# Kernel tuning notes

Measured on AMD Instinct MI355X. Metric: run time of the kernel, lower is better.

The kernel has to match this reference:

```python
import jax, jax.numpy as jnp
import numpy as np

PATCH = 32
K_FILT = 4
B, NP, C = 32, 256, 3


def _dct_matrix(n):
    i = np.arange(n)[:, None]
    j = np.arange(n)[None, :]
    scale = np.where(i == 0, np.sqrt(1.0 / n), np.sqrt(2.0 / n))
    m = scale * np.cos((j + 0.5) * np.pi * i / n)
    return jnp.asarray(m, dtype=jnp.float32)


def _bandpass_filters(n, k_filt):
    i = np.arange(n)[:, None]
    j = np.arange(n)[None, :]
    s = i + j  # [n, n]
    ks = np.arange(k_filt)[:, None, None]
    lo = 2.0 * n / k_filt * ks
    hi = 2.0 * n / k_filt * (ks + 1)
    f = ((s >= lo) & (s < hi)).astype(np.float32)  # [K, n, n]
    return jnp.asarray(f)


def setup_inputs() -> dict:
    key = jax.random.key(0)
    x = jax.random.normal(key, (B, NP, C, PATCH, PATCH), dtype=jnp.float32)
    return {
        'x': x,
        'dct_matrix': _dct_matrix(PATCH),
        'bandpass_filters': _bandpass_filters(PATCH, K_FILT),
    }


def reference(x, dct_matrix, bandpass_filters):
    # Batched 2D DCT: D @ patch @ D^T for every (b, n, c) patch.
    dct_coeffs = jnp.einsum('ih,bnchw,jw->bncij', dct_matrix, x, dct_matrix)
    log_abs = jnp.log1p(jnp.abs(dct_coeffs))  # log(|X| + 1)
    # patch_score = sum_k sum_c 2^k * (log_abs[c] * filter_k).sum()
    k_weights = 2.0 ** jnp.arange(bandpass_filters.shape[0], dtype=jnp.float32)
    weight_map = jnp.einsum('k,khw->hw', k_weights, bandpass_filters)  # [H, W]
    patch_grades = jnp.einsum('bnchw,hw->bn', log_abs, weight_map)
    return dct_coeffs, patch_grades
```

## Files before the change

kernel.cpp:

```cpp
#include <hip/hip_runtime.h>

#define NPIX 1024
#define CH   3
#define PPB  2
#define WVS  (PPB * CH)
#define BLK  (WVS * 64)

__global__ __launch_bounds__(BLK) void dct_grade_kernel(
    const float* __restrict__ x,
    const float* __restrict__ dct,
    float* __restrict__ out_coeffs,
    float* __restrict__ out_grades)
{
    __shared__ __align__(16) float Dt[NPIX];
    __shared__ __align__(16) float S[WVS][NPIX];
    __shared__ float partial[WVS];

    const int tid  = threadIdx.x;
    const int wid  = tid >> 6;
    const int lane = tid & 63;

    if (tid < 256) {
        int i  = tid & 31;
        int h0 = (tid >> 5) << 2;
        float4 dv = *reinterpret_cast<const float4*>(dct + i * 32 + h0);
        Dt[(h0 + 0) * 32 + i] = dv.x;
        Dt[(h0 + 1) * 32 + i] = dv.y;
        Dt[(h0 + 2) * 32 + i] = dv.z;
        Dt[(h0 + 3) * 32 + i] = dv.w;
    }
    __syncthreads();

    const int p  = (wid >= CH) ? 1 : 0;
    const int c  = wid - CH * p;
    const int pn = blockIdx.x * PPB + p;

    const int i0 = (lane >> 3) << 2;
    const int c0 = (lane & 7) << 2;
    const int sw = i0 ^ ((lane & 7) << 2);

    float* Sw = &S[wid][0];
    const float* xg   = x          + (size_t)pn * (CH * NPIX) + c * NPIX;
    float*       outp = out_coeffs + (size_t)pn * (CH * NPIX) + c * NPIX;

    {
        const float4* src = reinterpret_cast<const float4*>(xg);
        float4*       dst = reinterpret_cast<float4*>(Sw);
        #pragma unroll
        for (int k = 0; k < 4; ++k)
            dst[lane + 64 * k] = src[lane + 64 * k];
    }

    float acc[4][4];
    #pragma unroll
    for (int a = 0; a < 4; ++a)
        #pragma unroll
        for (int b = 0; b < 4; ++b) acc[a][b] = 0.0f;

    #pragma unroll
    for (int h = 0; h < 32; ++h) {
        float4 dv = *reinterpret_cast<const float4*>(&Dt[h * 32 + i0]);
        float4 xv = *reinterpret_cast<const float4*>(&Sw[h * 32 + c0]);
        float da[4] = {dv.x, dv.y, dv.z, dv.w};
        float xa[4] = {xv.x, xv.y, xv.z, xv.w};
        #pragma unroll
        for (int ii = 0; ii < 4; ++ii)
            #pragma unroll
            for (int ww = 0; ww < 4; ++ww)
                acc[ii][ww] += da[ii] * xa[ww];
    }

    #pragma unroll
    for (int ww = 0; ww < 4; ++ww) {
        float4 col = make_float4(acc[0][ww], acc[1][ww], acc[2][ww], acc[3][ww]);
        *reinterpret_cast<float4*>(&Sw[(c0 + ww) * 32 + sw]) = col;
    }

    float y[4][4];
    #pragma unroll
    for (int a = 0; a < 4; ++a)
        #pragma unroll
        for (int b = 0; b < 4; ++b) y[a][b] = 0.0f;

    #pragma unroll
    for (int w = 0; w < 32; ++w) {
        float4 tv = *reinterpret_cast<const float4*>(&Sw[w * 32 + (i0 ^ ((w >> 2) << 2))]);
        float4 dv = *reinterpret_cast<const float4*>(&Dt[w * 32 + c0]);
        float ta[4] = {tv.x, tv.y, tv.z, tv.w};
        float da[4] = {dv.x, dv.y, dv.z, dv.w};
        #pragma unroll
        for (int ii = 0; ii < 4; ++ii)
            #pragma unroll
            for (int jj = 0; jj < 4; ++jj)
                y[ii][jj] += ta[ii] * da[jj];
    }

    const int ssum = i0 + c0;
    float g = 0.0f;
    #pragma unroll
    for (int ii = 0; ii < 4; ++ii) {
        float4 st = make_float4(y[ii][0], y[ii][1], y[ii][2], y[ii][3]);
        *reinterpret_cast<float4*>(&outp[(i0 + ii) * 32 + c0]) = st;
        #pragma unroll
        for (int jj = 0; jj < 4; ++jj) {
            float wgt = (float)(1 << ((ssum + ii + jj) >> 4));
            g += __logf(1.0f + fabsf(y[ii][jj])) * wgt;
        }
    }

    #pragma unroll
    for (int off = 32; off > 0; off >>= 1)
        g += __shfl_down(g, off);
    if (lane == 0) partial[wid] = g;
    __syncthreads();
    if (tid < PPB)
        out_grades[blockIdx.x * PPB + tid] =
            partial[tid * CH + 0] + partial[tid * CH + 1] + partial[tid * CH + 2];
}

extern "C" void kernel_launch(void* const* d_in, const int* in_sizes, int n_in,
                              void* d_out, int out_size, void* d_ws, size_t ws_size,
                              hipStream_t stream) {
    const float* x   = (const float*)d_in[0];
    const float* dct = (const float*)d_in[1];
    float* out_coeffs = (float*)d_out;
    float* out_grades = (float*)d_out + (size_t)8192 * CH * NPIX;

    dct_grade_kernel<<<8192 / PPB, BLK, 0, stream>>>(x, dct, out_coeffs, out_grades);
}
```

Baseline: 190.0 us.

## Compute DCT per half-wave with register columns and padded LDS transpose

Each half-wave now handles one 32x32 channel slice: each lane loads one column of x into registers, computes the first DCT pass with DCT coefficients read from global memory (wave-uniform, likely scalar loads), and writes the result to an LDS tile padded to 33 columns. It then reads a row back and computes the second pass. The goal is to double the slices per block, drop the LDS staging of x and of the DCT matrix, and avoid bank conflicts. In exchange it uses more registers (64+ floats per lane), and the global stores become strided per-row float4 writes, which coalesce less well.

After: 220.4 us. 1.16x slower.

```diff
diff --git a/kernel.cpp b/kernel.cpp
--- a/kernel.cpp
+++ b/kernel.cpp
@@ -1,10 +1,11 @@
 #include <hip/hip_runtime.h>
 
-#define NPIX 1024
-#define CH   3
-#define PPB  2
-#define WVS  (PPB * CH)
-#define BLK  (WVS * 64)
+#define NPIX   1024
+#define CH     3
+#define WAVES  6
+#define SLICES (WAVES * 2)
+#define BLK    (WAVES * 64)
+#define LDP    33
 
 __global__ __launch_bounds__(BLK) void dct_grade_kernel(
     const float* __restrict__ x,
@@ -12,109 +13,80 @@
     float* __restrict__ out_coeffs,
     float* __restrict__ out_grades)
 {
-    __shared__ __align__(16) float Dt[NPIX];
-    __shared__ __align__(16) float S[WVS][NPIX];
-    __shared__ float partial[WVS];
+    __shared__ float T[SLICES][32 * LDP];
+    __shared__ float partial[SLICES];
 
     const int tid  = threadIdx.x;
     const int wid  = tid >> 6;
     const int lane = tid & 63;
+    const int half = lane >> 5;
+    const int t    = lane & 31;
 
-    if (tid < 256) {
-        int i  = tid & 31;
-        int h0 = (tid >> 5) << 2;
-        float4 dv = *reinterpret_cast<const float4*>(dct + i * 32 + h0);
-        Dt[(h0 + 0) * 32 + i] = dv.x;
-        Dt[(h0 + 1) * 32 + i] = dv.y;
-        Dt[(h0 + 2) * 32 + i] = dv.z;
-        Dt[(h0 + 3) * 32 + i] = dv.w;
-    }
-    __syncthreads();
+    const int slot = wid * 2 + half;
+    const int s    = blockIdx.x * SLICES + slot;
 
-    const int p  = (wid >= CH) ? 1 : 0;
-    const int c  = wid - CH * p;
-    const int pn = blockIdx.x * PPB + p;
+    const float* xg   = x          + (size_t)s * NPIX;
+    float*       outp = out_coeffs + (size_t)s * NPIX;
 
-    const int i0 = (lane >> 3) << 2;
-    const int c0 = (lane & 7) << 2;
-    const int sw = i0 ^ ((lane & 7) << 2);
+    float xcol[32];
+    #pragma unroll
+    for (int h = 0; h < 32; ++h)
+        xcol[h] = xg[h * 32 + t];
 
-    float* Sw = &S[wid][0];
-    const float* xg   = x          + (size_t)pn * (CH * NPIX) + c * NPIX;
-    float*       outp = out_coeffs + (size_t)pn * (CH * NPIX) + c * NPIX;
+    float* Tw = &T[slot][0];
 
-    {
-        const float4* src = reinterpret_cast<const float4*>(xg);
-        float4*       dst = reinterpret_cast<float4*>(Sw);
+    #pragma unroll
+    for (int i = 0; i < 32; ++i) {
+        const float* dr = dct + i * 32;
+        float p0 = 0.f, p1 = 0.f, p2 = 0.f, p3 = 0.f;
         #pragma unroll
-        for (int k = 0; k < 4; ++k)
-            dst[lane + 64 * k] = src[lane + 64 * k];
+        for (int h = 0; h < 32; h += 4) {
+            p0 += dr[h + 0] * xcol[h + 0];
+            p1 += dr[h + 1] * xcol[h + 1];
+            p2 += dr[h + 2] * xcol[h + 2];
+            p3 += dr[h + 3] * xcol[h + 3];
+        }
+        Tw[i * LDP + t] = (p0 + p1) + (p2 + p3);
     }
 
-    float acc[4][4];
+    float trow[32];
     #pragma unroll
-    for (int a = 0; a < 4; ++a)
-        #pragma unroll
-        for (int b = 0; b < 4; ++b) acc[a][b] = 0.0f;
+    for (int w = 0; w < 32; ++w)
+        trow[w] = Tw[t * LDP + w];
 
+    float g = 0.f;
     #pragma unroll
-    for (int h = 0; h < 32; ++h) {
-        float4 dv = *reinterpret_cast<const float4*>(&Dt[h * 32 + i0]);
-        float4 xv = *reinterpret_cast<const float4*>(&Sw[h * 32 + c0]);
-        float da[4] = {dv.x, dv.y, dv.z, dv.w};
-        float xa[4] = {xv.x, xv.y, xv.z, xv.w};
-        #pragma unroll
-        for (int ii = 0; ii < 4; ++ii)
-            #pragma unroll
-            for (int ww = 0; ww < 4; ++ww)
-                acc[ii][ww] += da[ii] * xa[ww];
-    }
-
-    #pragma unroll
-    for (int ww = 0; ww < 4; ++ww) {
-        float4 col = make_float4(acc[0][ww], acc[1][ww], acc[2][ww], acc[3][ww]);
-        *reinterpret_cast<float4*>(&Sw[(c0 + ww) * 32 + sw]) = col;
-    }
-
-    float y[4][4];
-    #pragma unroll
-    for (int a = 0; a < 4; ++a)
-        #pragma unroll
-        for (int b = 0; b < 4; ++b) y[a][b] = 0.0f;
-
-    #pragma unroll
-    for (int w = 0; w < 32; ++w) {
-        float4 tv = *reinterpret_cast<const float4*>(&Sw[w * 32 + (i0 ^ ((w >> 2) << 2))]);
-        float4 dv = *reinterpret_cast<const float4*>(&Dt[w * 32 + c0]);
-        float ta[4] = {tv.x, tv.y, tv.z, tv.w};
-        float da[4] = {dv.x, dv.y, dv.z, dv.w};
-        #pragma unroll
-        for (int ii = 0; ii < 4; ++ii)
-            #pragma unroll
-            for (int jj = 0; jj < 4; ++jj)
-                y[ii][jj] += ta[ii] * da[jj];
-    }
-
-    const int ssum = i0 + c0;
-    float g = 0.0f;
-    #pragma unroll
-    for (int ii = 0; ii < 4; ++ii) {
-        float4 st = make_float4(y[ii][0], y[ii][1], y[ii][2], y[ii][3]);
-        *reinterpret_cast<float4*>(&outp[(i0 + ii) * 32 + c0]) = st;
+    for (int j = 0; j < 32; j += 4) {
+        float y[4];
         #pragma unroll
         for (int jj = 0; jj < 4; ++jj) {
-            float wgt = (float)(1 << ((ssum + ii + jj) >> 4));
-            g += __logf(1.0f + fabsf(y[ii][jj])) * wgt;
+            const float* dr = dct + (j + jj) * 32;
+            float q0 = 0.f, q1 = 0.f, q2 = 0.f, q3 = 0.f;
+            #pragma unroll
+            for (int w = 0; w < 32; w += 4) {
+                q0 += dr[w + 0] * trow[w + 0];
+                q1 += dr[w + 1] * trow[w + 1];
+                q2 += dr[w + 2] * trow[w + 2];
+                q3 += dr[w + 3] * trow[w + 3];
+            }
+            y[jj] = (q0 + q1) + (q2 + q3);
+        }
+        *reinterpret_cast<float4*>(&outp[t * 32 + j]) =
+            make_float4(y[0], y[1], y[2], y[3]);
+        #pragma unroll
+        for (int jj = 0; jj < 4; ++jj) {
+            float wgt = (float)(1 << ((t + j + jj) >> 4));
+            g += __logf(1.0f + fabsf(y[jj])) * wgt;
         }
     }
 
     #pragma unroll
-    for (int off = 32; off > 0; off >>= 1)
-        g += __shfl_down(g, off);
-    if (lane == 0) partial[wid] = g;
+    for (int off = 16; off; off >>= 1)
+        g += __shfl_xor(g, off);
+    if (t == 0) partial[slot] = g;
     __syncthreads();
-    if (tid < PPB)
-        out_grades[blockIdx.x * PPB + tid] =
+    if (tid < SLICES / CH)
+        out_grades[blockIdx.x * (SLICES / CH) + tid] =
             partial[tid * CH + 0] + partial[tid * CH + 1] + partial[tid * CH + 2];
 }
 
@@ -126,5 +98,7 @@
     float* out_coeffs = (float*)d_out;
     float* out_grades = (float*)d_out + (size_t)8192 * CH * NPIX;
 
-    dct_grade_kernel<<<8192 / PPB, BLK, 0, stream>>>(x, dct, out_coeffs, out_grades);
+    const int n_slices = 8192 * CH;
+    dct_grade_kernel<<<n_slices / SLICES, BLK, 0, stream>>>(
+        x, dct, out_coeffs, out_grades);
 }
```

## Process four slices per wave with 8x8 register tiles and async LDS loads

Applied to the files above, without the earlier changes.

Restructures the kernel so each 16-lane group handles one channel slice with an 8x8 output tile per lane. A block now covers 16 slices with 4 waves, and the input is staged with global_load_lds direct-to-LDS copies. The intent is more FMA work per LDS read, fewer threads, and less register-staged loading. Per-patch grades are accumulated with atomicAdd after a memset, replacing the block-level shared reduction. In exchange it uses more shared memory and registers per thread, which can lower occupancy. It also drops the XOR swizzle, which may bring back LDS bank conflicts, and it makes the grade sum order nondeterministic.

Result: slower. 195.6 us (+3.0%).

```diff
diff --git a/kernel.cpp b/kernel.cpp
--- a/kernel.cpp
+++ b/kernel.cpp
@@ -2,9 +2,11 @@
 
 #define NPIX 1024
 #define CH   3
-#define PPB  2
-#define WVS  (PPB * CH)
-#define BLK  (WVS * 64)
+#define WPB  4
+#define SPW  4
+#define SPB  (WPB * SPW)
+#define BLK  (WPB * 64)
+#define LDP  1028
 
 __global__ __launch_bounds__(BLK) void dct_grade_kernel(
     const float* __restrict__ x,
@@ -13,16 +15,38 @@
     float* __restrict__ out_grades)
 {
     __shared__ __align__(16) float Dt[NPIX];
-    __shared__ __align__(16) float S[WVS][NPIX];
-    __shared__ float partial[WVS];
+    __shared__ __align__(16) float S[SPB][LDP];
 
     const int tid  = threadIdx.x;
     const int wid  = tid >> 6;
     const int lane = tid & 63;
+    const int sl   = lane >> 4;
+    const int u    = lane & 15;
+    const int i0   = (u >> 2) << 3;
+    const int c0   = (u & 3) << 3;
 
-    if (tid < 256) {
-        int i  = tid & 31;
-        int h0 = (tid >> 5) << 2;
+    const int slot = wid * SPW + sl;
+    const int sg   = blockIdx.x * SPB + slot;
+
+    {
+        const int ws0 = blockIdx.x * SPB + wid * SPW;
+        #pragma unroll
+        for (int q = 0; q < SPW; ++q) {
+            const float* gs = x + (size_t)(ws0 + q) * NPIX + lane * 4;
+            float*       ls = &S[wid * SPW + q][0];
+            #pragma unroll
+            for (int k = 0; k < 4; ++k) {
+                __builtin_amdgcn_global_load_lds(
+                    (const __attribute__((address_space(1))) void*)(gs + k * 256),
+                    (__attribute__((address_space(3))) void*)(ls + k * 256),
+                    16, 0, 0);
+            }
+        }
+    }
+
+    {
+        const int i  = tid & 31;
+        const int h0 = (tid >> 5) << 2;
         float4 dv = *reinterpret_cast<const float4*>(dct + i * 32 + h0);
         Dt[(h0 + 0) * 32 + i] = dv.x;
         Dt[(h0 + 1) * 32 + i] = dv.y;
@@ -31,91 +55,78 @@
     }
     __syncthreads();
 
-    const int p  = (wid >= CH) ? 1 : 0;
-    const int c  = wid - CH * p;
-    const int pn = blockIdx.x * PPB + p;
+    float* Sw = &S[slot][0];
 
-    const int i0 = (lane >> 3) << 2;
-    const int c0 = (lane & 7) << 2;
-    const int sw = i0 ^ ((lane & 7) << 2);
-
-    float* Sw = &S[wid][0];
-    const float* xg   = x          + (size_t)pn * (CH * NPIX) + c * NPIX;
-    float*       outp = out_coeffs + (size_t)pn * (CH * NPIX) + c * NPIX;
-
-    {
-        const float4* src = reinterpret_cast<const float4*>(xg);
-        float4*       dst = reinterpret_cast<float4*>(Sw);
+    float acc[8][8];
+    #pragma unroll
+    for (int a = 0; a < 8; ++a)
         #pragma unroll
-        for (int k = 0; k < 4; ++k)
-            dst[lane + 64 * k] = src[lane + 64 * k];
-    }
-
-    float acc[4][4];
-    #pragma unroll
-    for (int a = 0; a < 4; ++a)
-        #pragma unroll
-        for (int b = 0; b < 4; ++b) acc[a][b] = 0.0f;
+        for (int b = 0; b < 8; ++b) acc[a][b] = 0.0f;
 
     #pragma unroll
     for (int h = 0; h < 32; ++h) {
-        float4 dv = *reinterpret_cast<const float4*>(&Dt[h * 32 + i0]);
-        float4 xv = *reinterpret_cast<const float4*>(&Sw[h * 32 + c0]);
-        float da[4] = {dv.x, dv.y, dv.z, dv.w};
-        float xa[4] = {xv.x, xv.y, xv.z, xv.w};
+        float4 d0 = *reinterpret_cast<const float4*>(&Dt[h * 32 + i0]);
+        float4 d1 = *reinterpret_cast<const float4*>(&Dt[h * 32 + i0 + 4]);
+        float4 x0 = *reinterpret_cast<const float4*>(Sw + h * 32 + c0);
+        float4 x1 = *reinterpret_cast<const float4*>(Sw + h * 32 + c0 + 4);
+        float da[8] = {d0.x, d0.y, d0.z, d0.w, d1.x, d1.y, d1.z, d1.w};
+        float xa[8] = {x0.x, x0.y, x0.z, x0.w, x1.x, x1.y, x1.z, x1.w};
         #pragma unroll
-        for (int ii = 0; ii < 4; ++ii)
+        for (int a = 0; a < 8; ++a)
             #pragma unroll
-            for (int ww = 0; ww < 4; ++ww)
-                acc[ii][ww] += da[ii] * xa[ww];
+            for (int b = 0; b < 8; ++b)
+                acc[a][b] += da[a] * xa[b];
     }
 
     #pragma unroll
-    for (int ww = 0; ww < 4; ++ww) {
-        float4 col = make_float4(acc[0][ww], acc[1][ww], acc[2][ww], acc[3][ww]);
-        *reinterpret_cast<float4*>(&Sw[(c0 + ww) * 32 + sw]) = col;
+    for (int jj = 0; jj < 8; ++jj) {
+        *reinterpret_cast<float4*>(Sw + (c0 + jj) * 32 + i0) =
+            make_float4(acc[0][jj], acc[1][jj], acc[2][jj], acc[3][jj]);
+        *reinterpret_cast<float4*>(Sw + (c0 + jj) * 32 + i0 + 4) =
+            make_float4(acc[4][jj], acc[5][jj], acc[6][jj], acc[7][jj]);
     }
 
-    float y[4][4];
+    float y[8][8];
     #pragma unroll
-    for (int a = 0; a < 4; ++a)
+    for (int a = 0; a < 8; ++a)
         #pragma unroll
-        for (int b = 0; b < 4; ++b) y[a][b] = 0.0f;
+        for (int b = 0; b < 8; ++b) y[a][b] = 0.0f;
 
     #pragma unroll
     for (int w = 0; w < 32; ++w) {
-        float4 tv = *reinterpret_cast<const float4*>(&Sw[w * 32 + (i0 ^ ((w >> 2) << 2))]);
-        float4 dv = *reinterpret_cast<const float4*>(&Dt[w * 32 + c0]);
-        float ta[4] = {tv.x, tv.y, tv.z, tv.w};
-        float da[4] = {dv.x, dv.y, dv.z, dv.w};
+        float4 z0 = *reinterpret_cast<const float4*>(Sw + w * 32 + i0);
+        float4 z1 = *reinterpret_cast<const float4*>(Sw + w * 32 + i0 + 4);
+        float4 d0 = *reinterpret_cast<const float4*>(&Dt[w * 32 + c0]);
+        float4 d1 = *reinterpret_cast<const float4*>(&Dt[w * 32 + c0 + 4]);
+        float za[8] = {z0.x, z0.y, z0.z, z0.w, z1.x, z1.y, z1.z, z1.w};
+        float db[8] = {d0.x, d0.y, d0.z, d0.w, d1.x, d1.y, d1.z, d1.w};
         #pragma unroll
-        for (int ii = 0; ii < 4; ++ii)
+        for (int a = 0; a < 8; ++a)
             #pragma unroll
-            for (int jj = 0; jj < 4; ++jj)
-                y[ii][jj] += ta[ii] * da[jj];
+            for (int b = 0; b < 8; ++b)
+                y[a][b] += za[a] * db[b];
     }
 
-    const int ssum = i0 + c0;
+    float* outp = out_coeffs + (size_t)sg * NPIX;
     float g = 0.0f;
     #pragma unroll
-    for (int ii = 0; ii < 4; ++ii) {
-        float4 st = make_float4(y[ii][0], y[ii][1], y[ii][2], y[ii][3]);
-        *reinterpret_cast<float4*>(&outp[(i0 + ii) * 32 + c0]) = st;
+    for (int a = 0; a < 8; ++a) {
+        *reinterpret_cast<float4*>(outp + (i0 + a) * 32 + c0) =
+            make_float4(y[a][0], y[a][1], y[a][2], y[a][3]);
+        *reinterpret_cast<float4*>(outp + (i0 + a) * 32 + c0 + 4) =
+            make_float4(y[a][4], y[a][5], y[a][6], y[a][7]);
         #pragma unroll
-        for (int jj = 0; jj < 4; ++jj) {
-            float wgt = (float)(1 << ((ssum + ii + jj) >> 4));
-            g += __logf(1.0f + fabsf(y[ii][jj])) * wgt;
+        for (int b = 0; b < 8; ++b) {
+            float wgt = (float)(1 << ((i0 + a + c0 + b) >> 4));
+            g += __logf(1.0f + fabsf(y[a][b])) * wgt;
         }
     }
 
     #pragma unroll
-    for (int off = 32; off > 0; off >>= 1)
-        g += __shfl_down(g, off);
-    if (lane == 0) partial[wid] = g;
-    __syncthreads();
-    if (tid < PPB)
-        out_grades[blockIdx.x * PPB + tid] =
-            partial[tid * CH + 0] + partial[tid * CH + 1] + partial[tid * CH + 2];
+    for (int off = 1; off < 16; off <<= 1)
+        g += __shfl_xor(g, off);
+    if (u == 0)
+        atomicAdd(&out_grades[(unsigned)sg / 3u], g);
 }
 
 extern "C" void kernel_launch(void* const* d_in, const int* in_sizes, int n_in,
@@ -126,5 +137,9 @@
     float* out_coeffs = (float*)d_out;
     float* out_grades = (float*)d_out + (size_t)8192 * CH * NPIX;
 
-    dct_grade_kernel<<<8192 / PPB, BLK, 0, stream>>>(x, dct, out_coeffs, out_grades);
+    hipMemsetAsync(out_grades, 0, 8192 * sizeof(float), stream);
+
+    const int n_slices = 8192 * CH;
+    dct_grade_kernel<<<n_slices / SPB, BLK, 0, stream>>>(
+        x, dct, out_coeffs, out_grades);
 }
```
